# Kernel tuning notes

Hardware: AMD Instinct MI355X
Metric: run time of the kernel (lower is better)

Reference implementation:

```python
import math
import jax, jax.numpy as jnp
import numpy as np

WINDOW = 2  # LocalAttention default window_size
EPS = 1e-6


def _linear(x, W, b):
    return x @ W + b


def local_attention(x, Wq, bq, Wk, bk, Wv, bv):
    # x: [B, S, D]
    B, S, D = x.shape
    q = _linear(x, Wq, bq)
    k = _linear(x, Wk, bk)
    v = _linear(x, Wv, bv)
    idx = jnp.arange(S)
    # 0/1 banded mask -> softmax gives a dense row-stochastic matrix (faithful to source)
    mask = (jnp.abs(idx[:, None] - idx[None, :]) <= WINDOW).astype(x.dtype)  # [S, S]
    A = jax.nn.softmax(mask, axis=-1)  # [S, S]
    kk = jnp.einsum('st,btd->bsd', A, k)  # bmm(A, k)
    scores = jnp.einsum('bsd,btd->bst', q, kk) / math.sqrt(D)
    return jnp.einsum('bst,btd->bsd', jax.nn.softmax(scores, axis=-1), v)


def whole_norm(x, w, b):
    # LayerNorm with normalized_shape == full [B, S, D]: normalize over ALL elements
    mu = jnp.mean(x)
    var = jnp.mean(jnp.square(x - mu))
    return (x - mu) * jax.lax.rsqrt(var + EPS) * w + b


def ffn(x, W1, b1, W2, b2):
    return _linear(jax.nn.relu(_linear(x, W1, b1)), W2, b2)


def branch(feat, Wq, bq, Wk, bk, Wv, bv, W1, b1, W2, b2, nw, nb):
    out = local_attention(feat, Wq, bq, Wk, bk, Wv, bv)
    out = whole_norm(out + feat, nw, nb)
    out = ffn(out, W1, b1, W2, b2)
    return whole_norm(out + feat, nw, nb)


def _make_params(key, B, S, D):
    ks = jax.random.split(key, 5)
    s = 1.0 / math.sqrt(D)
    Wq = jax.random.normal(ks[0], (D, D), jnp.float32) * s
    Wk = jax.random.normal(ks[1], (D, D), jnp.float32) * s
    Wv = jax.random.normal(ks[2], (D, D), jnp.float32) * s
    W1 = jax.random.normal(ks[3], (D, 4 * D), jnp.float32) * s
    W2 = jax.random.normal(ks[4], (4 * D, D), jnp.float32) * (1.0 / math.sqrt(4 * D))
    return dict(Wq=Wq, bq=jnp.zeros((D,)), Wk=Wk, bk=jnp.zeros((D,)),
                Wv=Wv, bv=jnp.zeros((D,)), W1=W1, b1=jnp.zeros((4 * D,)),
                W2=W2, b2=jnp.zeros((D,)), nw=jnp.ones((B, S, D)), nb=jnp.zeros((B, S, D)))


def setup_inputs() -> dict:
    key = jax.random.key(0)
    k0, k1, k2, k3 = jax.random.split(key, 4)
    B, St, Dt = 8, 512, 1024
    Si, Di = 196, 768
    inp = {
        'text_feature': jax.random.normal(k0, (B, St, Dt), jnp.float32),
        'image_feature': jax.random.normal(k1, (B, Si, Di), jnp.float32),
    }
    tp = _make_params(k2, B, St, Dt)
    ip = _make_params(k3, B, Si, Di)
    for k, v in tp.items():
        inp['t_' + k] = v
    for k, v in ip.items():
        inp['i_' + k] = v
    return inp


def reference(text_feature, image_feature,
              t_Wq, t_bq, t_Wk, t_bk, t_Wv, t_bv, t_W1, t_b1, t_W2, t_b2, t_nw, t_nb,
              i_Wq, i_bq, i_Wk, i_bk, i_Wv, i_bv, i_W1, i_b1, i_W2, i_b2, i_nw, i_nb):
    image_out = branch(image_feature, i_Wq, i_bq, i_Wk, i_bk, i_Wv, i_bv,
                       i_W1, i_b1, i_W2, i_b2, i_nw, i_nb)
    text_out = branch(text_feature, t_Wq, t_bq, t_Wk, t_bk, t_Wv, t_bv,
                      t_W1, t_b1, t_W2, t_b2, t_nw, t_nb)
    return (text_out, image_out)
```

## Files before the change

kernel.cpp:

```cpp
#include <hip/hip_runtime.h>
#include <math.h>

typedef float  f32x4  __attribute__((ext_vector_type(4)));
typedef short  bf16x8 __attribute__((ext_vector_type(8)));

__device__ __forceinline__ unsigned short f2bf(float f) {
    union { float f; unsigned u; } v; v.f = f;
    unsigned u = v.u;
    return (unsigned short)((u + 0x7FFFu + ((u >> 16) & 1u)) >> 16);
}
__device__ __forceinline__ float bf2f(unsigned short u) {
    union { unsigned u; float f; } v; v.u = (unsigned)u << 16; return v.f;
}

#define GLOAD_LDS16(g, l)                                                      \
    __builtin_amdgcn_global_load_lds(                                          \
        (const __attribute__((address_space(1))) void*)(g),                    \
        (__attribute__((address_space(3))) void*)(l), 16, 0, 0)

template<int NR, bool OUT_BF16, bool RELU>
__global__ __launch_bounds__(512, 2)
void gemm3_bf16(const unsigned short* __restrict__ A,
                const unsigned short* __restrict__ BT,
                const float* __restrict__ bias, void* __restrict__ Cv,
                int M, int N, int K, int lda, int ldb, int ldc,
                long long sA, long long sB, long long sC, float alpha,
                int gx, int gy)
{
    constexpr int MR = 8;
    constexpr int BK = 64;
    constexpr int BM = 256, BN = NR * 64;
    constexpr int WN = NR * 16;
    __shared__ unsigned short Asm[2][BM * BK];
    __shared__ unsigned short Bsm[2][BN * BK];

    A  += (long long)blockIdx.z * sA;
    BT += (long long)blockIdx.z * sB;
    char* Cb = (char*)Cv + (long long)blockIdx.z * sC * (OUT_BF16 ? 2 : 4);

    const int nwg = gx * gy;
    int orig = blockIdx.x;
    int xcd = orig & 7, sidx = orig >> 3;
    int qq = nwg >> 3, rr = nwg & 7;
    int wg = (xcd < rr ? xcd * (qq + 1) : rr * (qq + 1) + (xcd - rr) * qq) + sidx;
    const int row0 = (wg / gx) * BM;
    const int col0 = (wg % gx) * BN;

    const int tid  = threadIdx.x;
    const int lane = tid & 63;
    const int wave = tid >> 6;
    const int wr   = wave >> 2;
    const int wc   = wave & 3;

    const int lrow = lane & 15;
    const int cgrp = lane >> 4;

    f32x4 acc[MR][NR] = {};

    const int srl = tid >> 3;
    const int scl = (tid & 7) ^ (srl & 7);

    auto stage = [&](int buf, int k0) {
        #pragma unroll
        for (int is = 0; is < BM / 64; ++is)
            GLOAD_LDS16(A + (long long)(row0 + is * 64 + srl) * lda + (k0 + scl * 8),
                        &Asm[buf][is * 64 * BK + tid * 8]);
        #pragma unroll
        for (int is = 0; is < BN / 64; ++is)
            GLOAD_LDS16(BT + (long long)(col0 + is * 64 + srl) * ldb + (k0 + scl * 8),
                        &Bsm[buf][is * 64 * BK + tid * 8]);
    };

    const int nt = K / BK;
    stage(0, 0);
    __syncthreads();

    for (int t = 0; t < nt; ++t) {
        if (t + 1 < nt) stage((t + 1) & 1, (t + 1) * BK);
        const int cur = t & 1;

        #pragma unroll
        for (int kk = 0; kk < 2; ++kk) {
            bf16x8 a_[MR];
            #pragma unroll
            for (int mf = 0; mf < MR; ++mf) {
                int row = wr * 128 + mf * 16 + lrow;
                int phys = (kk * 4 + cgrp) ^ (row & 7);
                a_[mf] = *(const bf16x8*)&Asm[cur][row * BK + phys * 8];
            }
            bf16x8 b_[NR];
            #pragma unroll
            for (int nf = 0; nf < NR; ++nf) {
                int row = wc * WN + nf * 16 + lrow;
                int phys = (kk * 4 + cgrp) ^ (row & 7);
                b_[nf] = *(const bf16x8*)&Bsm[cur][row * BK + phys * 8];
            }
            #pragma unroll
            for (int mf = 0; mf < MR; ++mf)
                #pragma unroll
                for (int nf = 0; nf < NR; ++nf)
                    acc[mf][nf] = __builtin_amdgcn_mfma_f32_16x16x32_bf16(
                        a_[mf], b_[nf], acc[mf][nf], 0, 0, 0);
        }
        __syncthreads();
    }

    const int crow = cgrp * 4;
    const int ccol = lane & 15;
    #pragma unroll
    for (int mf = 0; mf < MR; ++mf) {
        int rbase = row0 + wr * 128 + mf * 16 + crow;
        #pragma unroll
        for (int nf = 0; nf < NR; ++nf) {
            int c = col0 + wc * WN + nf * 16 + ccol;
            if (c >= N) continue;
            float bv = bias ? bias[c] : 0.f;
            #pragma unroll
            for (int j = 0; j < 4; ++j) {
                int r = rbase + j;
                if (r >= M) continue;
                float v = acc[mf][nf][j] * alpha + bv;
                if (RELU) v = fmaxf(v, 0.f);
                if (OUT_BF16)
                    ((unsigned short*)Cb)[(long long)r * ldc + c] = f2bf(v);
                else
                    ((float*)Cb)[(long long)r * ldc + c] = v;
            }
        }
    }
}

template<int NR>
static void gemm3_t(bool outBf16, bool relu,
                    const unsigned short* A, const unsigned short* BT, const float* bias,
                    void* C, int M, int N, int K, int lda, int ldb, int ldc,
                    int batch, long long sA, long long sB, long long sC,
                    float alpha, hipStream_t st)
{
    const int BM = 256, BN = NR * 64;
    int gx = (N + BN - 1) / BN, gy = (M + BM - 1) / BM;
    dim3 grid(gx * gy, 1, batch);
    if (outBf16) {
        if (relu) gemm3_bf16<NR, true , true ><<<grid, 512, 0, st>>>(A, BT, bias, C, M, N, K, lda, ldb, ldc, sA, sB, sC, alpha, gx, gy);
        else      gemm3_bf16<NR, true , false><<<grid, 512, 0, st>>>(A, BT, bias, C, M, N, K, lda, ldb, ldc, sA, sB, sC, alpha, gx, gy);
    } else {
        if (relu) gemm3_bf16<NR, false, true ><<<grid, 512, 0, st>>>(A, BT, bias, C, M, N, K, lda, ldb, ldc, sA, sB, sC, alpha, gx, gy);
        else      gemm3_bf16<NR, false, false><<<grid, 512, 0, st>>>(A, BT, bias, C, M, N, K, lda, ldb, ldc, sA, sB, sC, alpha, gx, gy);
    }
}

template<int MR, int NR, bool OUT_BF16, bool RELU>
__global__ __launch_bounds__(512, 4)
void gemm2_bf16(const unsigned short* __restrict__ A,
                const unsigned short* __restrict__ BT,
                const float* __restrict__ bias, void* __restrict__ Cv,
                int M, int N, int K, int lda, int ldb, int ldc,
                long long sA, long long sB, long long sC, float alpha,
                int gx, int gy)
{
    constexpr int BK = 32;
    constexpr int WM = MR * 16, WN = NR * 16;
    constexpr int BM = 2 * WM, BN = 4 * WN;
    __shared__ unsigned short Asm[2][BM * BK];
    __shared__ unsigned short Bsm[2][BN * BK];

    A  += (long long)blockIdx.z * sA;
    BT += (long long)blockIdx.z * sB;
    char* Cb = (char*)Cv + (long long)blockIdx.z * sC * (OUT_BF16 ? 2 : 4);

    const int nwg = gx * gy;
    int orig = blockIdx.x;
    int xcd = orig & 7, sidx = orig >> 3;
    int qq = nwg >> 3, rr = nwg & 7;
    int wg = (xcd < rr ? xcd * (qq + 1) : rr * (qq + 1) + (xcd - rr) * qq) + sidx;
    const int row0 = (wg / gx) * BM;
    const int col0 = (wg % gx) * BN;

    const int tid  = threadIdx.x;
    const int lane = tid & 63;
    const int wave = tid >> 6;
    const int wr   = wave >> 2;
    const int wc   = wave & 3;

    const int srow = tid >> 2;
    const int skel = (tid & 3) * 8;

    const int lrow = lane & 15;
    const int lk   = (lane >> 4) * 8;

    f32x4 acc[MR][NR] = {};

    auto stage = [&](int buf, int k0) {
        #pragma unroll
        for (int is = 0; is < BM / 128; ++is)
            GLOAD_LDS16(A + (long long)(row0 + is * 128 + srow) * lda + (k0 + skel),
                        &Asm[buf][(is * 128 + srow) * BK + skel]);
        #pragma unroll
        for (int is = 0; is < BN / 128; ++is)
            GLOAD_LDS16(BT + (long long)(col0 + is * 128 + srow) * ldb + (k0 + skel),
                        &Bsm[buf][(is * 128 + srow) * BK + skel]);
    };

    const int nt = K / BK;
    stage(0, 0);
    __syncthreads();
    int cur = 0;
    for (int t = 0; t < nt; ++t) {
        if (t + 1 < nt) stage(cur ^ 1, (t + 1) * BK);

        bf16x8 af[MR], bfr[NR];
        #pragma unroll
        for (int mf = 0; mf < MR; ++mf)
            af[mf] = *(const bf16x8*)&Asm[cur][(wr * WM + mf * 16 + lrow) * BK + lk];
        #pragma unroll
        for (int nf = 0; nf < NR; ++nf)
            bfr[nf] = *(const bf16x8*)&Bsm[cur][(wc * WN + nf * 16 + lrow) * BK + lk];
        #pragma unroll
        for (int mf = 0; mf < MR; ++mf)
            #pragma unroll
            for (int nf = 0; nf < NR; ++nf)
                acc[mf][nf] = __builtin_amdgcn_mfma_f32_16x16x32_bf16(
                    af[mf], bfr[nf], acc[mf][nf], 0, 0, 0);

        __syncthreads();
        cur ^= 1;
    }

    const int crow = (lane >> 4) * 4;
    const int ccol = lane & 15;
    #pragma unroll
    for (int mf = 0; mf < MR; ++mf) {
        int rbase = row0 + wr * WM + mf * 16 + crow;
        #pragma unroll
        for (int nf = 0; nf < NR; ++nf) {
            int c = col0 + wc * WN + nf * 16 + ccol;
            if (c >= N) continue;
            float bv = bias ? bias[c] : 0.f;
            #pragma unroll
            for (int j = 0; j < 4; ++j) {
                int r = rbase + j;
                if (r >= M) continue;
                float v = acc[mf][nf][j] * alpha + bv;
                if (RELU) v = fmaxf(v, 0.f);
                if (OUT_BF16)
                    ((unsigned short*)Cb)[(long long)r * ldc + c] = f2bf(v);
                else
                    ((float*)Cb)[(long long)r * ldc + c] = v;
            }
        }
    }
}

template<int MR, int NR>
static void gemm2_t(bool outBf16, bool relu,
                    const unsigned short* A, const unsigned short* BT, const float* bias,
                    void* C, int M, int N, int K, int lda, int ldb, int ldc,
                    int batch, long long sA, long long sB, long long sC,
                    float alpha, hipStream_t st)
{
    const int BM = 2 * MR * 16, BN = 4 * NR * 16;
    int gx = (N + BN - 1) / BN, gy = (M + BM - 1) / BM;
    dim3 grid(gx * gy, 1, batch);
    if (outBf16) {
        if (relu) gemm2_bf16<MR, NR, true , true ><<<grid, 512, 0, st>>>(A, BT, bias, C, M, N, K, lda, ldb, ldc, sA, sB, sC, alpha, gx, gy);
        else      gemm2_bf16<MR, NR, true , false><<<grid, 512, 0, st>>>(A, BT, bias, C, M, N, K, lda, ldb, ldc, sA, sB, sC, alpha, gx, gy);
    } else {
        if (relu) gemm2_bf16<MR, NR, false, true ><<<grid, 512, 0, st>>>(A, BT, bias, C, M, N, K, lda, ldb, ldc, sA, sB, sC, alpha, gx, gy);
        else      gemm2_bf16<MR, NR, false, false><<<grid, 512, 0, st>>>(A, BT, bias, C, M, N, K, lda, ldb, ldc, sA, sB, sC, alpha, gx, gy);
    }
}

template<int BM, int BN, bool OUT_BF16>
__global__ __launch_bounds__(256)
void gemm_bf16(const unsigned short* __restrict__ A,
               const unsigned short* __restrict__ BT,
               const float* __restrict__ bias, void* __restrict__ Cv,
               int M, int N, int K, int lda, int ldb, int ldc,
               long long sA, long long sB, long long sC, float alpha,
               int gx, int gy)
{
    constexpr int BK = 32;
    constexpr int WM = BM / 2, WN = BN / 2;
    constexpr int MR = WM / 16, NR = WN / 16;
    __shared__ unsigned short Asm[BM * BK];
    __shared__ unsigned short Bsm[BN * BK];

    A  += (long long)blockIdx.z * sA;
    BT += (long long)blockIdx.z * sB;
    char* Cb = (char*)Cv + (long long)blockIdx.z * sC * (OUT_BF16 ? 2 : 4);

    const int nwg = gx * gy;
    int orig = blockIdx.x;
    int xcd = orig & 7, sidx = orig >> 3;
    int qq = nwg >> 3, rr = nwg & 7;
    int wg = (xcd < rr ? xcd * (qq + 1) : rr * (qq + 1) + (xcd - rr) * qq) + sidx;
    const int row0 = (wg % gy) * BM;
    const int col0 = (wg / gy) * BN;

    const int tid  = threadIdx.x;
    const int lane = tid & 63;
    const int wave = tid >> 6;
    const int wr   = wave >> 1;
    const int wc   = wave & 1;

    const int srow = tid >> 2;
    const int skel = (tid & 3) * 8;

    f32x4 acc[MR][NR] = {};

    const int lrow = lane & 15;
    const int lk   = (lane >> 4) * 8;

    for (int k0 = 0; k0 < K; k0 += BK) {
        #pragma unroll
        for (int is = 0; is < BM / 64; ++is)
            GLOAD_LDS16(A + (long long)(row0 + is * 64 + srow) * lda + (k0 + skel),
                        &Asm[(is * 64 + srow) * BK + skel]);
        #pragma unroll
        for (int is = 0; is < BN / 64; ++is)
            GLOAD_LDS16(BT + (long long)(col0 + is * 64 + srow) * ldb + (k0 + skel),
                        &Bsm[(is * 64 + srow) * BK + skel]);
        __syncthreads();

        bf16x8 af[MR], bfr[NR];
        #pragma unroll
        for (int mf = 0; mf < MR; ++mf)
            af[mf] = *(const bf16x8*)&Asm[(wr * WM + mf * 16 + lrow) * BK + lk];
        #pragma unroll
        for (int nf = 0; nf < NR; ++nf)
            bfr[nf] = *(const bf16x8*)&Bsm[(wc * WN + nf * 16 + lrow) * BK + lk];
        #pragma unroll
        for (int mf = 0; mf < MR; ++mf)
            #pragma unroll
            for (int nf = 0; nf < NR; ++nf)
                acc[mf][nf] = __builtin_amdgcn_mfma_f32_16x16x32_bf16(
                    af[mf], bfr[nf], acc[mf][nf], 0, 0, 0);
        __syncthreads();
    }

    const int crow = (lane >> 4) * 4;
    const int ccol = lane & 15;
    #pragma unroll
    for (int mf = 0; mf < MR; ++mf) {
        int rbase = row0 + wr * WM + mf * 16 + crow;
        #pragma unroll
        for (int nf = 0; nf < NR; ++nf) {
            int c = col0 + wc * WN + nf * 16 + ccol;
            if (c >= N) continue;
            float bv = bias ? bias[c] : 0.f;
            #pragma unroll
            for (int j = 0; j < 4; ++j) {
                int r = rbase + j;
                if (r >= M) continue;
                float v = acc[mf][nf][j] * alpha + bv;
                if (OUT_BF16)
                    ((unsigned short*)Cb)[(long long)r * ldc + c] = f2bf(v);
                else
                    ((float*)Cb)[(long long)r * ldc + c] = v;
            }
        }
    }
}

template<int BM, int BN>
static void gemm_t(bool outBf16,
                   const unsigned short* A, const unsigned short* BT, const float* bias,
                   void* C, int M, int N, int K, int lda, int ldb, int ldc,
                   int batch, long long sA, long long sB, long long sC,
                   float alpha, hipStream_t st)
{
    int gx = (N + BN - 1) / BN, gy = (M + BM - 1) / BM;
    dim3 grid(gx * gy, 1, batch);
    if (outBf16)
        gemm_bf16<BM, BN, true ><<<grid, 256, 0, st>>>(A, BT, bias, C, M, N, K, lda, ldb, ldc, sA, sB, sC, alpha, gx, gy);
    else
        gemm_bf16<BM, BN, false><<<grid, 256, 0, st>>>(A, BT, bias, C, M, N, K, lda, ldb, ldc, sA, sB, sC, alpha, gx, gy);
}

__global__ void splitk_stats_kernel(const float4* __restrict__ part,
                                    const float4* __restrict__ bias,
                                    const float4* __restrict__ x,
                                    float4* __restrict__ z,
                                    double* __restrict__ dpart,
                                    long long n4, int N4, int nsplit, long long stride4)
{
    __shared__ double rs[256], rs2[256];
    int tid = threadIdx.x;
    long long i = (long long)blockIdx.x * blockDim.x + tid;
    long long gs = (long long)gridDim.x * blockDim.x;
    double s = 0.0, s2 = 0.0;
    for (; i < n4; i += gs) {
        float4 a = part[i];
        for (int sp = 1; sp < nsplit; ++sp) {
            float4 b = part[(long long)sp * stride4 + i];
            a.x += b.x; a.y += b.y; a.z += b.z; a.w += b.w;
        }
        float4 bv = bias[(int)(i % N4)];
        float4 xv = x[i];
        a.x += bv.x + xv.x; a.y += bv.y + xv.y; a.z += bv.z + xv.z; a.w += bv.w + xv.w;
        z[i] = a;
        s  += (double)a.x + (double)a.y + (double)a.z + (double)a.w;
        s2 += (double)a.x * a.x + (double)a.y * a.y + (double)a.z * a.z + (double)a.w * a.w;
    }
    rs[tid] = s; rs2[tid] = s2; __syncthreads();
    for (int k = 128; k > 0; k >>= 1) {
        if (tid < k) { rs[tid] += rs[tid + k]; rs2[tid] += rs2[tid + k]; }
        __syncthreads();
    }
    if (tid == 0) { dpart[2 * blockIdx.x] = rs[0]; dpart[2 * blockIdx.x + 1] = rs2[0]; }
}

__global__ void norm_apply_z_kernel(const float4* __restrict__ z,
                                    const float4* __restrict__ nw, const float4* __restrict__ nb,
                                    const float* __restrict__ stats, float4* __restrict__ out,
                                    long long n4)
{
    float mu = stats[0], rstd = stats[1];
    long long i = (long long)blockIdx.x * blockDim.x + threadIdx.x;
    long long stride = (long long)gridDim.x * blockDim.x;
    for (; i < n4; i += stride) {
        float4 zv = z[i], wv = nw[i], bv = nb[i];
        float4 o;
        o.x = (zv.x - mu) * rstd * wv.x + bv.x;
        o.y = (zv.y - mu) * rstd * wv.y + bv.y;
        o.z = (zv.z - mu) * rstd * wv.z + bv.z;
        o.w = (zv.w - mu) * rstd * wv.w + bv.w;
        out[i] = o;
    }
}

__global__ void cast_bf16_kernel(const float4* __restrict__ in,
                                 ushort4* __restrict__ out, long long n4)
{
    long long i = (long long)blockIdx.x * blockDim.x + threadIdx.x;
    long long stride = (long long)gridDim.x * blockDim.x;
    for (; i < n4; i += stride) {
        float4 v = in[i];
        ushort4 o;
        o.x = f2bf(v.x); o.y = f2bf(v.y); o.z = f2bf(v.z); o.w = f2bf(v.w);
        out[i] = o;
    }
}

__global__ void transpose_cast_kernel(const float* __restrict__ src,
                                      unsigned short* __restrict__ dst,
                                      int R, int C, int Rpad,
                                      long long sSrc, long long sDst)
{
    __shared__ float t[32][33];
    src += (long long)blockIdx.z * sSrc;
    dst += (long long)blockIdx.z * sDst;
    int r0 = blockIdx.x * 32, c0 = blockIdx.y * 32;
    int tx = threadIdx.x & 31, ty = threadIdx.x >> 5;
    #pragma unroll
    for (int i = 0; i < 32; i += 8) {
        int r = r0 + ty + i, c = c0 + tx;
        t[ty + i][tx] = (r < R && c < C) ? src[(long long)r * C + c] : 0.f;
    }
    __syncthreads();
    #pragma unroll
    for (int i = 0; i < 32; i += 8) {
        int c = c0 + ty + i, r = r0 + tx;
        if (c < C && r < Rpad)
            dst[(long long)c * Rpad + r] = f2bf(t[tx][ty + i]);
    }
}

__global__ void transpose_bf16_kernel(const unsigned short* __restrict__ src,
                                      unsigned short* __restrict__ dst,
                                      int R, int C, int Rpad, int ldS,
                                      long long sSrc, long long sDst)
{
    __shared__ unsigned short t[32][33];
    src += (long long)blockIdx.z * sSrc;
    dst += (long long)blockIdx.z * sDst;
    int r0 = blockIdx.x * 32, c0 = blockIdx.y * 32;
    int tx = threadIdx.x & 31, ty = threadIdx.x >> 5;
    #pragma unroll
    for (int i = 0; i < 32; i += 8) {
        int r = r0 + ty + i, c = c0 + tx;
        t[ty + i][tx] = (r < R && c < C) ? src[(long long)r * ldS + c] : (unsigned short)0;
    }
    __syncthreads();
    #pragma unroll
    for (int i = 0; i < 32; i += 8) {
        int c = c0 + ty + i, r = r0 + tx;
        if (c < C && r < Rpad)
            dst[(long long)c * Rpad + r] = t[tx][ty + i];
    }
}

#define KTOT_NCH 16
__global__ void ktot_partial_bf16(const unsigned short* __restrict__ k,
                                  float* __restrict__ part,
                                  int B, int S, int D, int ld)
{
    int bch = blockIdx.x;
    int b  = bch / KTOT_NCH;
    int ch = bch % KTOT_NCH;
    int d  = blockIdx.y * 256 + threadIdx.x;
    if (d >= D) return;
    int len = (S + KTOT_NCH - 1) / KTOT_NCH;
    int lo = ch * len;
    int hi = lo + len < S ? lo + len : S;
    const unsigned short* kp = k + ((long long)b * S + lo) * ld + d;
    float s = 0.f;
    for (int t = lo; t < hi; ++t, kp += ld) s += bf2f(*kp);
    part[(long long)bch * D + d] = s;
}

__global__ void ktot_finish_kernel(const float* __restrict__ part,
                                   float* __restrict__ ktot, int B, int D)
{
    int idx = blockIdx.x * blockDim.x + threadIdx.x;
    if (idx >= B * D) return;
    int b = idx / D, d = idx % D;
    float s = 0.f;
    #pragma unroll
    for (int ch = 0; ch < KTOT_NCH; ++ch)
        s += part[((long long)b * KTOT_NCH + ch) * D + d];
    ktot[idx] = s;
}

__global__ void kk_bf16_kernel(const unsigned short* __restrict__ k,
                               const float* __restrict__ ktot,
                               unsigned short* __restrict__ kk,
                               int B, int S, int D, int ld)
{
    long long idx = (long long)blockIdx.x * blockDim.x + threadIdx.x;
    int D4 = D >> 2;
    long long n4 = (long long)B * S * D4;
    if (idx >= n4) return;
    int d4 = (int)(idx % D4);
    long long bs = idx / D4;
    int s = (int)(bs % S);
    int b = (int)(bs / S);
    int lo = s - 2 > 0 ? s - 2 : 0;
    int hi = s + 2 < S - 1 ? s + 2 : S - 1;
    int c = hi - lo + 1;
    const float E = 2.718281828459045f;
    float Zinv = 1.f / ((float)(S - c) + E * (float)c);

    float w0 = 0.f, w1 = 0.f, w2 = 0.f, w3 = 0.f;
    const unsigned short* kp = k + ((long long)b * S + lo) * ld + d4 * 4;
    for (int t = lo; t <= hi; ++t, kp += ld) {
        ushort4 kv = *(const ushort4*)kp;
        w0 += bf2f(kv.x); w1 += bf2f(kv.y); w2 += bf2f(kv.z); w3 += bf2f(kv.w);
    }
    float4 tot = *((const float4*)(ktot + b * D) + d4);
    ushort4 o;
    o.x = f2bf((tot.x + (E - 1.f) * w0) * Zinv);
    o.y = f2bf((tot.y + (E - 1.f) * w1) * Zinv);
    o.z = f2bf((tot.z + (E - 1.f) * w2) * Zinv);
    o.w = f2bf((tot.w + (E - 1.f) * w3) * Zinv);
    ((ushort4*)(kk + ((long long)b * S + s) * D))[d4] = o;
}

__global__ void softmax_rows_bf16(const float* __restrict__ sc,
                                  unsigned short* __restrict__ P, int S, int Spad)
{
    long long row = blockIdx.x;
    const float* p = sc + row * (long long)Spad;
    unsigned short* o = P + row * (long long)Spad;
    int tid = threadIdx.x;
    __shared__ float red[256];

    float m = -INFINITY;
    for (int t = tid; t < S; t += 256) m = fmaxf(m, p[t]);
    red[tid] = m; __syncthreads();
    for (int s = 128; s > 0; s >>= 1) {
        if (tid < s) red[tid] = fmaxf(red[tid], red[tid + s]);
        __syncthreads();
    }
    m = red[0];
    __syncthreads();

    float sum = 0.f;
    for (int t = tid; t < S; t += 256) sum += __expf(p[t] - m);
    red[tid] = sum; __syncthreads();
    for (int s = 128; s > 0; s >>= 1) {
        if (tid < s) red[tid] += red[tid + s];
        __syncthreads();
    }
    float inv = 1.f / red[0];
    for (int t = tid; t < Spad; t += 256)
        o[t] = (t < S) ? f2bf(__expf(p[t] - m) * inv) : (unsigned short)0;
}

__global__ void stats_kernel(const float4* __restrict__ a, const float4* __restrict__ f,
                             double* __restrict__ part, long long n4)
{
    __shared__ double rs[256], rs2[256];
    int tid = threadIdx.x;
    long long i = (long long)blockIdx.x * blockDim.x + tid;
    long long stride = (long long)gridDim.x * blockDim.x;
    double s = 0.0, s2 = 0.0;
    for (; i < n4; i += stride) {
        float4 av = a[i], fv = f[i];
        float z0 = av.x + fv.x, z1 = av.y + fv.y, z2 = av.z + fv.z, z3 = av.w + fv.w;
        s  += (double)z0 + (double)z1 + (double)z2 + (double)z3;
        s2 += (double)z0 * z0 + (double)z1 * z1 + (double)z2 * z2 + (double)z3 * z3;
    }
    rs[tid] = s; rs2[tid] = s2; __syncthreads();
    for (int k = 128; k > 0; k >>= 1) {
        if (tid < k) { rs[tid] += rs[tid + k]; rs2[tid] += rs2[tid + k]; }
        __syncthreads();
    }
    if (tid == 0) { part[2 * blockIdx.x] = rs[0]; part[2 * blockIdx.x + 1] = rs2[0]; }
}

__global__ void finish_stats(const double* __restrict__ part, int npart,
                             float* __restrict__ stats, double n)
{
    __shared__ double rs[256], rs2[256];
    int tid = threadIdx.x;
    double s = 0.0, s2 = 0.0;
    for (int i = tid; i < npart; i += 256) { s += part[2 * i]; s2 += part[2 * i + 1]; }
    rs[tid] = s; rs2[tid] = s2; __syncthreads();
    for (int k = 128; k > 0; k >>= 1) {
        if (tid < k) { rs[tid] += rs[tid + k]; rs2[tid] += rs2[tid + k]; }
        __syncthreads();
    }
    if (tid == 0) {
        double mu  = rs[0] / n;
        double var = rs2[0] / n - mu * mu;
        stats[0] = (float)mu;
        stats[1] = (float)(1.0 / sqrt(var + 1e-6));
    }
}

__global__ void norm_apply_kernel(const float4* __restrict__ a, const float4* __restrict__ f,
                                  const float4* __restrict__ nw, const float4* __restrict__ nb,
                                  const float* __restrict__ stats, ushort4* __restrict__ out,
                                  long long n4)
{
    float mu = stats[0], rstd = stats[1];
    long long i = (long long)blockIdx.x * blockDim.x + threadIdx.x;
    long long stride = (long long)gridDim.x * blockDim.x;
    for (; i < n4; i += stride) {
        float4 av = a[i], fv = f[i], wv = nw[i], bv = nb[i];
        ushort4 o;
        o.x = f2bf((av.x + fv.x - mu) * rstd * wv.x + bv.x);
        o.y = f2bf((av.y + fv.y - mu) * rstd * wv.y + bv.y);
        o.z = f2bf((av.z + fv.z - mu) * rstd * wv.z + bv.z);
        o.w = f2bf((av.w + fv.w - mu) * rstd * wv.w + bv.w);
        out[i] = o;
    }
}

struct Bufs {
    unsigned short *xb, *qkv, *kkb, *vT, *P, *h, *WqkvT, *W1T, *W2T;
    float *f32buf, *bqkv, *ktot, *ktot_part, *stats;
    double *part;
};

static void run_branch(const float* x, const float* const* w, bool big,
                       float* out, int B, int S, int D, const Bufs& wsb, hipStream_t st)
{
    const float *Wq = w[0], *bq = w[1], *Wk = w[2], *bk = w[3], *Wv = w[4], *bv = w[5];
    const float *W1 = w[6], *b1 = w[7], *W2 = w[8], *b2 = w[9], *nw = w[10], *nb = w[11];

    const int Spad = (S + 31) & ~31;
    const long long M = (long long)B * S;
    const long long n = M * D;
    const long long n4 = n / 4;
    const float inv_sqrt_d = (float)(1.0 / sqrt((double)D));
    const int D3 = 3 * D, D4 = 4 * D;

    unsigned short* y1b = wsb.kkb;
    float* scores = (float*)wsb.h;
    float* splitbuf = (float*)wsb.qkv;

    cast_bf16_kernel<<<1024, 256, 0, st>>>((const float4*)x, (ushort4*)wsb.xb, n4);
    transpose_cast_kernel<<<dim3((D + 31) / 32, (D + 31) / 32, 1), 256, 0, st>>>(Wq, wsb.WqkvT,               D, D, D, 0, 0);
    transpose_cast_kernel<<<dim3((D + 31) / 32, (D + 31) / 32, 1), 256, 0, st>>>(Wk, wsb.WqkvT + (long long)D * D, D, D, D, 0, 0);
    transpose_cast_kernel<<<dim3((D + 31) / 32, (D + 31) / 32, 1), 256, 0, st>>>(Wv, wsb.WqkvT + 2LL * D * D, D, D, D, 0, 0);
    transpose_cast_kernel<<<dim3((D + 31) / 32, (D4 + 31) / 32, 1), 256, 0, st>>>(W1, wsb.W1T, D, D4, D, 0, 0);
    transpose_cast_kernel<<<dim3((D4 + 31) / 32, (D + 31) / 32, 1), 256, 0, st>>>(W2, wsb.W2T, D4, D, D4, 0, 0);
    hipMemcpyAsync(wsb.bqkv,         bq, D * sizeof(float), hipMemcpyDeviceToDevice, st);
    hipMemcpyAsync(wsb.bqkv + D,     bk, D * sizeof(float), hipMemcpyDeviceToDevice, st);
    hipMemcpyAsync(wsb.bqkv + 2 * D, bv, D * sizeof(float), hipMemcpyDeviceToDevice, st);

    if (big)
        gemm3_t<4>(true, false, wsb.xb, wsb.WqkvT, wsb.bqkv, wsb.qkv,
                   (int)M, D3, D, D, D, D3, 1, 0, 0, 0, 1.f, st);
    else
        gemm2_t<4, 2>(true, false, wsb.xb, wsb.WqkvT, wsb.bqkv, wsb.qkv,
                      (int)M, D3, D, D, D, D3, 1, 0, 0, 0, 1.f, st);

    const unsigned short* kcol = wsb.qkv + D;
    ktot_partial_bf16<<<dim3(B * KTOT_NCH, (D + 255) / 256), 256, 0, st>>>(kcol, wsb.ktot_part, B, S, D, D3);
    ktot_finish_kernel<<<(B * D + 255) / 256, 256, 0, st>>>(wsb.ktot_part, wsb.ktot, B, D);
    kk_bf16_kernel<<<(int)((n4 + 255) / 256), 256, 0, st>>>(kcol, wsb.ktot, wsb.kkb, B, S, D, D3);

    transpose_bf16_kernel<<<dim3((Spad + 31) / 32, (D + 31) / 32, B), 256, 0, st>>>(
        wsb.qkv + 2 * D, wsb.vT, S, D, Spad, D3, (long long)S * D3, (long long)D * Spad);

    gemm_t<64, 64>(false, wsb.qkv, wsb.kkb, nullptr, scores, S, S, D, D3, D, Spad,
                   B, (long long)S * D3, (long long)S * D, (long long)S * Spad, inv_sqrt_d, st);
    softmax_rows_bf16<<<(int)M, 256, 0, st>>>(scores, wsb.P, S, Spad);

    gemm_t<128, 64>(false, wsb.P, wsb.vT, nullptr, wsb.f32buf, S, D, Spad, Spad, Spad, D,
                    B, (long long)S * Spad, (long long)D * Spad, (long long)S * D, 1.f, st);

    stats_kernel<<<1024, 256, 0, st>>>((const float4*)wsb.f32buf, (const float4*)x, wsb.part, n4);
    finish_stats<<<1, 256, 0, st>>>(wsb.part, 1024, wsb.stats, (double)n);
    norm_apply_kernel<<<2048, 256, 0, st>>>((const float4*)wsb.f32buf, (const float4*)x,
        (const float4*)nw, (const float4*)nb, wsb.stats, (ushort4*)y1b, n4);

    if (big)
        gemm3_t<4>(true, true, y1b, wsb.W1T, b1, wsb.h, (int)M, D4, D, D, D, D4, 1, 0, 0, 0, 1.f, st);
    else
        gemm2_t<4, 2>(true, true, y1b, wsb.W1T, b1, wsb.h, (int)M, D4, D, D, D, D4, 1, 0, 0, 0, 1.f, st);

    {
        int nsplit = big ? 2 : 8;
        int Ksp = D4 / nsplit;
        if (big)
            gemm3_t<2>(false, false, wsb.h, wsb.W2T, nullptr, splitbuf,
                       (int)M, D, Ksp, D4, D4, D,
                       nsplit, Ksp, Ksp, M * D, 1.f, st);
        else
            gemm2_t<4, 2>(false, false, wsb.h, wsb.W2T, nullptr, splitbuf,
                          (int)M, D, Ksp, D4, D4, D,
                          nsplit, Ksp, Ksp, M * D, 1.f, st);
        splitk_stats_kernel<<<1024, 256, 0, st>>>((const float4*)splitbuf, (const float4*)b2,
                                                  (const float4*)x, (float4*)wsb.f32buf,
                                                  wsb.part, n4, D / 4, nsplit, n4);
        finish_stats<<<1, 256, 0, st>>>(wsb.part, 1024, wsb.stats, (double)n);
        norm_apply_z_kernel<<<2048, 256, 0, st>>>((const float4*)wsb.f32buf,
            (const float4*)nw, (const float4*)nb, wsb.stats, (float4*)out, n4);
    }
}

extern "C" void kernel_launch(void* const* d_in, const int* in_sizes, int n_in,
                              void* d_out, int out_size, void* d_ws, size_t ws_size,
                              hipStream_t stream)
{
    const float* text  = (const float*)d_in[0];
    const float* image = (const float*)d_in[1];
    const float* tw[12];
    const float* iw[12];
    for (int i = 0; i < 12; ++i) tw[i] = (const float*)d_in[2 + i];
    for (int i = 0; i < 12; ++i) iw[i] = (const float*)d_in[14 + i];

    float* out_text = (float*)d_out;
    float* out_img  = out_text + 8LL * 512 * 1024;

    char* p = (char*)d_ws;
    auto alloc = [&](long long bytes) {
        char* r = p;
        p += (bytes + 255) & ~255LL;
        return r;
    };
    const long long MD  = 4096LL * 1024;
    const long long BDS = 8LL * 1024 * 512;
    const long long SS  = 8LL * 512 * 512;
    Bufs b;
    b.xb      = (unsigned short*)alloc(MD * 2);
    b.qkv     = (unsigned short*)alloc(MD * 3 * 2);
    b.kkb     = (unsigned short*)alloc(MD * 2);
    b.vT      = (unsigned short*)alloc(BDS * 2);
    b.P       = (unsigned short*)alloc(SS * 2);
    b.h       = (unsigned short*)alloc(MD * 4 * 2);
    b.WqkvT   = (unsigned short*)alloc(3LL * 1024 * 1024 * 2);
    b.W1T     = (unsigned short*)alloc(4096LL * 1024 * 2);
    b.W2T     = (unsigned short*)alloc(4096LL * 1024 * 2);
    b.f32buf  = (float*)alloc(MD * 4);
    b.bqkv    = (float*)alloc(3LL * 1024 * 4);
    b.ktot    = (float*)alloc(8192LL * 4);
    b.ktot_part = (float*)alloc(8192LL * KTOT_NCH * 4);
    b.part    = (double*)alloc(2048LL * 8);
    b.stats   = (float*)alloc(256);

    run_branch(text,  tw, true,  out_text, 8, 512, 1024, b, stream);
    run_branch(image, iw, false, out_img,  8, 196, 768,  b, stream);
}
```

Measured before the change: 483.1 us.

## Pipeline GEMM loads with partial vmcnt waits, generalize warp layout, widen small-GEMM BK

```diff
diff --git a/kernel.cpp b/kernel.cpp
--- a/kernel.cpp
+++ b/kernel.cpp
@@ -18,19 +18,19 @@
         (const __attribute__((address_space(1))) void*)(g),                    \
         (__attribute__((address_space(3))) void*)(l), 16, 0, 0)
 
-template<int NR, bool OUT_BF16, bool RELU>
+template<int WRW, int WCW, int MR, int NR, bool OUT_BF16, bool RELU>
 __global__ __launch_bounds__(512, 2)
-void gemm3_bf16(const unsigned short* __restrict__ A,
+void gemm5_bf16(const unsigned short* __restrict__ A,
                 const unsigned short* __restrict__ BT,
                 const float* __restrict__ bias, void* __restrict__ Cv,
                 int M, int N, int K, int lda, int ldb, int ldc,
                 long long sA, long long sB, long long sC, float alpha,
                 int gx, int gy)
 {
-    constexpr int MR = 8;
     constexpr int BK = 64;
-    constexpr int BM = 256, BN = NR * 64;
-    constexpr int WN = NR * 16;
+    constexpr int WM = MR * 16, WN = NR * 16;
+    constexpr int BM = WRW * WM, BN = WCW * WN;
+    constexpr int NL = (BM + BN) / 64;
     __shared__ unsigned short Asm[2][BM * BK];
     __shared__ unsigned short Bsm[2][BN * BK];
 
@@ -49,8 +49,8 @@
     const int tid  = threadIdx.x;
     const int lane = tid & 63;
     const int wave = tid >> 6;
-    const int wr   = wave >> 2;
-    const int wc   = wave & 3;
+    const int wr   = wave / WCW;
+    const int wc   = wave % WCW;
 
     const int lrow = lane & 15;
     const int cgrp = lane >> 4;
@@ -73,43 +73,52 @@
 
     const int nt = K / BK;
     stage(0, 0);
-    __syncthreads();
 
     for (int t = 0; t < nt; ++t) {
-        if (t + 1 < nt) stage((t + 1) & 1, (t + 1) * BK);
         const int cur = t & 1;
+        if (t + 1 < nt) {
+            stage(cur ^ 1, (t + 1) * BK);
+            if constexpr (NL == 8)      asm volatile("s_waitcnt vmcnt(8)" ::: "memory");
+            else if constexpr (NL == 6) asm volatile("s_waitcnt vmcnt(6)" ::: "memory");
+            else                        asm volatile("s_waitcnt vmcnt(0)" ::: "memory");
+        } else {
+            asm volatile("s_waitcnt vmcnt(0)" ::: "memory");
+        }
+        __builtin_amdgcn_s_barrier();
+        __builtin_amdgcn_sched_barrier(0);
 
         #pragma unroll
         for (int kk = 0; kk < 2; ++kk) {
-            bf16x8 a_[MR];
+            bf16x8 a_[MR], b_[NR];
             #pragma unroll
             for (int mf = 0; mf < MR; ++mf) {
-                int row = wr * 128 + mf * 16 + lrow;
+                int row = wr * WM + mf * 16 + lrow;
                 int phys = (kk * 4 + cgrp) ^ (row & 7);
                 a_[mf] = *(const bf16x8*)&Asm[cur][row * BK + phys * 8];
             }
-            bf16x8 b_[NR];
             #pragma unroll
             for (int nf = 0; nf < NR; ++nf) {
                 int row = wc * WN + nf * 16 + lrow;
                 int phys = (kk * 4 + cgrp) ^ (row & 7);
                 b_[nf] = *(const bf16x8*)&Bsm[cur][row * BK + phys * 8];
             }
+            __builtin_amdgcn_s_setprio(1);
             #pragma unroll
             for (int mf = 0; mf < MR; ++mf)
                 #pragma unroll
                 for (int nf = 0; nf < NR; ++nf)
                     acc[mf][nf] = __builtin_amdgcn_mfma_f32_16x16x32_bf16(
                         a_[mf], b_[nf], acc[mf][nf], 0, 0, 0);
+            __builtin_amdgcn_s_setprio(0);
         }
-        __syncthreads();
+        __builtin_amdgcn_s_barrier();
     }
 
     const int crow = cgrp * 4;
     const int ccol = lane & 15;
     #pragma unroll
     for (int mf = 0; mf < MR; ++mf) {
-        int rbase = row0 + wr * 128 + mf * 16 + crow;
+        int rbase = row0 + wr * WM + mf * 16 + crow;
         #pragma unroll
         for (int nf = 0; nf < NR; ++nf) {
             int c = col0 + wc * WN + nf * 16 + ccol;
@@ -130,35 +139,35 @@
     }
 }
 
-template<int NR>
-static void gemm3_t(bool outBf16, bool relu,
+template<int WRW, int WCW, int MR, int NR>
+static void gemm5_t(bool outBf16, bool relu,
                     const unsigned short* A, const unsigned short* BT, const float* bias,
                     void* C, int M, int N, int K, int lda, int ldb, int ldc,
                     int batch, long long sA, long long sB, long long sC,
                     float alpha, hipStream_t st)
 {
-    const int BM = 256, BN = NR * 64;
+    const int BM = WRW * MR * 16, BN = WCW * NR * 16;
     int gx = (N + BN - 1) / BN, gy = (M + BM - 1) / BM;
     dim3 grid(gx * gy, 1, batch);
     if (outBf16) {
-        if (relu) gemm3_bf16<NR, true , true ><<<grid, 512, 0, st>>>(A, BT, bias, C, M, N, K, lda, ldb, ldc, sA, sB, sC, alpha, gx, gy);
-        else      gemm3_bf16<NR, true , false><<<grid, 512, 0, st>>>(A, BT, bias, C, M, N, K, lda, ldb, ldc, sA, sB, sC, alpha, gx, gy);
+        if (relu) gemm5_bf16<WRW, WCW, MR, NR, true , true ><<<grid, 512, 0, st>>>(A, BT, bias, C, M, N, K, lda, ldb, ldc, sA, sB, sC, alpha, gx, gy);
+        else      gemm5_bf16<WRW, WCW, MR, NR, true , false><<<grid, 512, 0, st>>>(A, BT, bias, C, M, N, K, lda, ldb, ldc, sA, sB, sC, alpha, gx, gy);
     } else {
-        if (relu) gemm3_bf16<NR, false, true ><<<grid, 512, 0, st>>>(A, BT, bias, C, M, N, K, lda, ldb, ldc, sA, sB, sC, alpha, gx, gy);
-        else      gemm3_bf16<NR, false, false><<<grid, 512, 0, st>>>(A, BT, bias, C, M, N, K, lda, ldb, ldc, sA, sB, sC, alpha, gx, gy);
+        if (relu) gemm5_bf16<WRW, WCW, MR, NR, false, true ><<<grid, 512, 0, st>>>(A, BT, bias, C, M, N, K, lda, ldb, ldc, sA, sB, sC, alpha, gx, gy);
+        else      gemm5_bf16<WRW, WCW, MR, NR, false, false><<<grid, 512, 0, st>>>(A, BT, bias, C, M, N, K, lda, ldb, ldc, sA, sB, sC, alpha, gx, gy);
     }
 }
 
 template<int MR, int NR, bool OUT_BF16, bool RELU>
 __global__ __launch_bounds__(512, 4)
-void gemm2_bf16(const unsigned short* __restrict__ A,
+void gemm4_bf16(const unsigned short* __restrict__ A,
                 const unsigned short* __restrict__ BT,
                 const float* __restrict__ bias, void* __restrict__ Cv,
                 int M, int N, int K, int lda, int ldb, int ldc,
                 long long sA, long long sB, long long sC, float alpha,
                 int gx, int gy)
 {
-    constexpr int BK = 32;
+    constexpr int BK = 64;
     constexpr int WM = MR * 16, WN = NR * 16;
     constexpr int BM = 2 * WM, BN = 4 * WN;
     __shared__ unsigned short Asm[2][BM * BK];
@@ -182,51 +191,65 @@
     const int wr   = wave >> 2;
     const int wc   = wave & 3;
 
-    const int srow = tid >> 2;
-    const int skel = (tid & 3) * 8;
-
     const int lrow = lane & 15;
-    const int lk   = (lane >> 4) * 8;
+    const int cgrp = lane >> 4;
 
     f32x4 acc[MR][NR] = {};
 
+    const int srl = tid >> 3;
+    const int scl = (tid & 7) ^ (srl & 7);
+
     auto stage = [&](int buf, int k0) {
         #pragma unroll
-        for (int is = 0; is < BM / 128; ++is)
-            GLOAD_LDS16(A + (long long)(row0 + is * 128 + srow) * lda + (k0 + skel),
-                        &Asm[buf][(is * 128 + srow) * BK + skel]);
-        #pragma unroll
-        for (int is = 0; is < BN / 128; ++is)
-            GLOAD_LDS16(BT + (long long)(col0 + is * 128 + srow) * ldb + (k0 + skel),
-                        &Bsm[buf][(is * 128 + srow) * BK + skel]);
+        for (int is = 0; is < BM / 64; ++is)
+            GLOAD_LDS16(A + (long long)(row0 + is * 64 + srl) * lda + (k0 + scl * 8),
+                        &Asm[buf][is * 64 * BK + tid * 8]);
+        #pragma unroll
+        for (int is = 0; is < BN / 64; ++is)
+            GLOAD_LDS16(BT + (long long)(col0 + is * 64 + srl) * ldb + (k0 + scl * 8),
+                        &Bsm[buf][is * 64 * BK + tid * 8]);
     };
 
     const int nt = K / BK;
     stage(0, 0);
     __syncthreads();
-    int cur = 0;
+
     for (int t = 0; t < nt; ++t) {
-        if (t + 1 < nt) stage(cur ^ 1, (t + 1) * BK);
-
-        bf16x8 af[MR], bfr[NR];
-        #pragma unroll
-        for (int mf = 0; mf < MR; ++mf)
-            af[mf] = *(const bf16x8*)&Asm[cur][(wr * WM + mf * 16 + lrow) * BK + lk];
-        #pragma unroll
-        for (int nf = 0; nf < NR; ++nf)
-            bfr[nf] = *(const bf16x8*)&Bsm[cur][(wc * WN + nf * 16 + lrow) * BK + lk];
-        #pragma unroll
-        for (int mf = 0; mf < MR; ++mf)
-            #pragma unroll
-            for (int nf = 0; nf < NR; ++nf)
-                acc[mf][nf] = __builtin_amdgcn_mfma_f32_16x16x32_bf16(
-                    af[mf], bfr[nf], acc[mf][nf], 0, 0, 0);
+        if (t + 1 < nt) stage((t + 1) & 1, (t + 1) * BK);
+        const int cur = t & 1;
+
+        bf16x8 a_[2][MR], b_[2][NR];
+        #pragma unroll
+        for (int kk = 0; kk < 2; ++kk) {
+            #pragma unroll
+            for (int mf = 0; mf < MR; ++mf) {
+                int row = wr * WM + mf * 16 + lrow;
+                int phys = (kk * 4 + cgrp) ^ (row & 7);
+                a_[kk][mf] = *(const bf16x8*)&Asm[cur][row * BK + phys * 8];
+            }
+            #pragma unroll
+            for (int nf = 0; nf < NR; ++nf) {
+                int row = wc * WN + nf * 16 + lrow;
+                int phys = (kk * 4 + cgrp) ^ (row & 7);
+                b_[kk][nf] = *(const bf16x8*)&Bsm[cur][row * BK + phys * 8];
+            }
+        }
+
+        __builtin_amdgcn_s_setprio(1);
+        #pragma unroll
+        for (int kk = 0; kk < 2; ++kk)
+            #pragma unroll
+            for (int mf = 0; mf < MR; ++mf)
+                #pragma unroll
+                for (int nf = 0; nf < NR; ++nf)
+                    acc[mf][nf] = __builtin_amdgcn_mfma_f32_16x16x32_bf16(
+                        a_[kk][mf], b_[kk][nf], acc[mf][nf], 0, 0, 0);
+        __builtin_amdgcn_s_setprio(0);
 
         __syncthreads();
-        cur ^= 1;
-    }
-
-    const int crow = (lane >> 4) * 4;
+    }
+
+    const int crow = cgrp * 4;
     const int ccol = lane & 15;
     #pragma unroll
     for (int mf = 0; mf < MR; ++mf) {
@@ -252,7 +275,7 @@
 }
 
 template<int MR, int NR>
-static void gemm2_t(bool outBf16, bool relu,
+static void gemm4_t(bool outBf16, bool relu,
                     const unsigned short* A, const unsigned short* BT, const float* bias,
                     void* C, int M, int N, int K, int lda, int ldb, int ldc,
                     int batch, long long sA, long long sB, long long sC,
@@ -262,11 +285,11 @@
     int gx = (N + BN - 1) / BN, gy = (M + BM - 1) / BM;
     dim3 grid(gx * gy, 1, batch);
     if (outBf16) {
-        if (relu) gemm2_bf16<MR, NR, true , true ><<<grid, 512, 0, st>>>(A, BT, bias, C, M, N, K, lda, ldb, ldc, sA, sB, sC, alpha, gx, gy);
-        else      gemm2_bf16<MR, NR, true , false><<<grid, 512, 0, st>>>(A, BT, bias, C, M, N, K, lda, ldb, ldc, sA, sB, sC, alpha, gx, gy);
+        if (relu) gemm4_bf16<MR, NR, true , true ><<<grid, 512, 0, st>>>(A, BT, bias, C, M, N, K, lda, ldb, ldc, sA, sB, sC, alpha, gx, gy);
+        else      gemm4_bf16<MR, NR, true , false><<<grid, 512, 0, st>>>(A, BT, bias, C, M, N, K, lda, ldb, ldc, sA, sB, sC, alpha, gx, gy);
     } else {
-        if (relu) gemm2_bf16<MR, NR, false, true ><<<grid, 512, 0, st>>>(A, BT, bias, C, M, N, K, lda, ldb, ldc, sA, sB, sC, alpha, gx, gy);
-        else      gemm2_bf16<MR, NR, false, false><<<grid, 512, 0, st>>>(A, BT, bias, C, M, N, K, lda, ldb, ldc, sA, sB, sC, alpha, gx, gy);
+        if (relu) gemm4_bf16<MR, NR, false, true ><<<grid, 512, 0, st>>>(A, BT, bias, C, M, N, K, lda, ldb, ldc, sA, sB, sC, alpha, gx, gy);
+        else      gemm4_bf16<MR, NR, false, false><<<grid, 512, 0, st>>>(A, BT, bias, C, M, N, K, lda, ldb, ldc, sA, sB, sC, alpha, gx, gy);
     }
 }
 
@@ -682,10 +705,10 @@
     hipMemcpyAsync(wsb.bqkv + 2 * D, bv, D * sizeof(float), hipMemcpyDeviceToDevice, st);
 
     if (big)
-        gemm3_t<4>(true, false, wsb.xb, wsb.WqkvT, wsb.bqkv, wsb.qkv,
-                   (int)M, D3, D, D, D, D3, 1, 0, 0, 0, 1.f, st);
+        gemm5_t<2, 4, 8, 4>(true, false, wsb.xb, wsb.WqkvT, wsb.bqkv, wsb.qkv,
+                            (int)M, D3, D, D, D, D3, 1, 0, 0, 0, 1.f, st);
     else
-        gemm2_t<4, 2>(true, false, wsb.xb, wsb.WqkvT, wsb.bqkv, wsb.qkv,
+        gemm4_t<4, 2>(true, false, wsb.xb, wsb.WqkvT, wsb.bqkv, wsb.qkv,
                       (int)M, D3, D, D, D, D3, 1, 0, 0, 0, 1.f, st);
 
     const unsigned short* kcol = wsb.qkv + D;
@@ -709,19 +732,20 @@
         (const float4*)nw, (const float4*)nb, wsb.stats, (ushort4*)y1b, n4);
 
     if (big)
-        gemm3_t<4>(true, true, y1b, wsb.W1T, b1, wsb.h, (int)M, D4, D, D, D, D4, 1, 0, 0, 0, 1.f, st);
+        gemm5_t<2, 4, 8, 4>(true, true, y1b, wsb.W1T, b1, wsb.h,
+                            (int)M, D4, D, D, D, D4, 1, 0, 0, 0, 1.f, st);
     else
-        gemm2_t<4, 2>(true, true, y1b, wsb.W1T, b1, wsb.h, (int)M, D4, D, D, D, D4, 1, 0, 0, 0, 1.f, st);
+        gemm4_t<4, 2>(true, true, y1b, wsb.W1T, b1, wsb.h, (int)M, D4, D, D, D, D4, 1, 0, 0, 0, 1.f, st);
 
     {
         int nsplit = big ? 2 : 8;
         int Ksp = D4 / nsplit;
         if (big)
-            gemm3_t<2>(false, false, wsb.h, wsb.W2T, nullptr, splitbuf,
-                       (int)M, D, Ksp, D4, D4, D,
-                       nsplit, Ksp, Ksp, M * D, 1.f, st);
+            gemm5_t<4, 2, 4, 4>(false, false, wsb.h, wsb.W2T, nullptr, splitbuf,
+                                (int)M, D, Ksp, D4, D4, D,
+                                nsplit, Ksp, Ksp, M * D, 1.f, st);
         else
-            gemm2_t<4, 2>(false, false, wsb.h, wsb.W2T, nullptr, splitbuf,
+            gemm4_t<4, 2>(false, false, wsb.h, wsb.W2T, nullptr, splitbuf,
                           (int)M, D, Ksp, D4, D4, D,
                           nsplit, Ksp, Ksp, M * D, 1.f, st);
         splitk_stats_kernel<<<1024, 256, 0, st>>>((const float4*)splitbuf, (const float4*)b2,
```

Result: no change. 491.5 us (+1.7%).
